# Optimization experiments

Hardware: AMD Instinct MI355X
Metric: run time of the kernel (lower is better)

Reference implementation:

```python
import jax, jax.numpy as jnp
import numpy as np

V = 25; NE = 5; DIM = 192; H = 6; HD = 32; N = 64; T = 64
SCALE = HD ** -0.5
COEFF = 0.4
NTU_EDGES = [(1,2),(2,21),(3,21),(4,3),(5,21),(6,5),(7,6),(8,7),(9,21),(10,9),(11,10),(12,11),(13,1),(14,13),(15,14),(16,15),(17,1),(18,17),(19,18),(20,19),(22,23),(23,8),(24,25),(25,12)]

def _compute_hops():
    # replicate MHSA.__init__ hop-distance computation (A = [I, adj, adj] summed+binarized)
    adj = np.zeros((V, V))
    for i, j in NTU_EDGES:
        adj[i-1, j-1] = 1.0; adj[j-1, i-1] = 1.0
    h1 = ((np.eye(V) + adj) != 0).astype(np.float64)
    h = [None] * V
    h[0] = np.eye(V); h[1] = h1
    hops = np.zeros((V, V))
    for i in range(2, V):
        h[i] = ((h[i-1] @ h1.T) != 0).astype(np.float64)
    for i in range(V-1, 0, -1):
        if np.any(h[i] - h[i-1]):
            h[i] = h[i] - h[i-1]
            hops += i * h[i]
    return hops.astype(np.int32)

def setup_inputs() -> dict:
    key = jax.random.key(0)
    ks = jax.random.split(key, 12)
    hops = jnp.asarray(_compute_hops())
    n_hop = int(hops.max()) + 1
    std = 0.02
    return {
        "x": jax.random.normal(ks[0], (N, DIM, T, V), jnp.float32),
        "joint_label": jnp.arange(V, dtype=jnp.int32) % NE,  # all 5 hyperedge labels present
        "groups": NE,  # unused by forward (kept for signature fidelity)
        "he_weight": jax.random.uniform(ks[1], (NE,), jnp.float32),
        "hops": hops,
        "ln_g": jnp.ones((DIM,), jnp.float32),
        "ln_b": jnp.zeros((DIM,), jnp.float32),
        "hgc_w": std * jax.random.normal(ks[2], (DIM, DIM), jnp.float32),
        "q_w": std * jax.random.normal(ks[3], (DIM, DIM), jnp.float32),
        "kv_w": std * jax.random.normal(ks[4], (2 * DIM, DIM), jnp.float32),
        "proj_w": std * jax.random.normal(ks[5], (DIM, HD), jnp.float32),  # grouped 1x1 conv, groups=6
        "proj_b": jnp.zeros((DIM,), jnp.float32),
        "rpe": std * jax.random.normal(ks[6], (n_hop, DIM), jnp.float32),
        "w1": std * jax.random.normal(ks[7], (H, HD), jnp.float32),
        "outer": jnp.tile(jnp.eye(V, dtype=jnp.float32), (H, 1, 1)) + std * jax.random.normal(ks[8], (H, V, V), jnp.float32),
        "alpha": 0.1 * jnp.ones((1,), jnp.float32),
        "lin1_w": std * jax.random.normal(ks[9], (T // 5, T), jnp.float32),
        "lin1_b": jnp.zeros((T // 5,), jnp.float32),
        "lin2_w": std * jax.random.normal(ks[10], (T, T // 5), jnp.float32),
        "lin2_b": jnp.zeros((T,), jnp.float32),
    }

def _forward(x, joint_label, he_weight, hops, ln_g, ln_b, hgc_w, q_w, kv_w, proj_w, proj_b, rpe, w1, outer, alpha, lin1_w, lin1_b, lin2_w, lin2_b):
    N_, C, T_, V_ = x.shape
    # ---- HGattn branch: hypergraph conv + temporal squeeze-excite gate ----
    label = jax.nn.one_hot(joint_label, NE, dtype=x.dtype)            # (V, 5)
    label1 = label / label.sum(0, keepdims=True)
    label1 = label1 / jnp.sqrt(label.sum(1, keepdims=True))
    label1 = (he_weight[None, :] * label1).T                          # (5, V)
    norm_label = label / label.sum(1, keepdims=True)
    h_adj = norm_label @ label1                                       # (V, V)
    z = jnp.einsum('nctv,vw->nctw', x, h_adj)
    op = jnp.einsum('nctv,oc->notv', z, hgc_w)                        # (N, dim, T, V) 1x1 conv
    op_tr = op.transpose(0, 1, 3, 2)                                  # (N, dim, V, T)
    s = op_tr.mean(axis=(1, 2))                                       # (N, T) global avg pool over (dim, V)
    g = jax.nn.sigmoid(jax.nn.relu(s @ lin1_w.T + lin1_b) @ lin2_w.T + lin2_b)  # (N, T)
    op_final = op_tr + COEFF * (op_tr * g[:, None, None, :])
    e = op_final.transpose(0, 1, 3, 2)                                # (N, dim, T, V)
    # ---- LayerNorm over channel dim ----
    xc = x.transpose(0, 2, 3, 1)                                      # (N, T, V, C)
    mu = xc.mean(-1, keepdims=True)
    var = xc.var(-1, keepdims=True)
    xn = (((xc - mu) / jnp.sqrt(var + 1e-5)) * ln_g + ln_b).transpose(0, 3, 1, 2)
    # ---- MHSA with hop-indexed relative bias, e-branch scores, outer fusion ----
    q = jnp.einsum('nctv,oc->notv', xn, q_w).reshape(N_, H, HD, T_, V_).transpose(0, 3, 1, 4, 2)   # (N,T,H,V,hd)
    kv = jnp.einsum('nctv,oc->notv', xn, kv_w).reshape(N_, 2, H, HD, T_, V_)
    k = kv[:, 0].transpose(0, 3, 1, 4, 2)
    v = kv[:, 1].transpose(0, 3, 1, 4, 2)
    e_k = e.reshape(N_, H, HD, T_, V_).transpose(0, 3, 1, 4, 2)
    k_r = rpe[hops].reshape(V_, V_, H, HD)                            # hop-distance relative position table
    b = jnp.einsum('bthnc,nmhc->bthnm', q, k_r)
    c = jnp.einsum('bthnc,bthmc->bthnm', q, e_k)
    d = jnp.einsum('hc,bthmc->bthm', w1, e_k)[..., None, :]
    a = jnp.einsum('bthnc,bthmc->bthnm', q, k)
    attn = jax.nn.softmax((a + b + c + d) * SCALE, axis=-1)
    o = jnp.einsum('bthnm,bthmc->bthnc', alpha * attn + outer[None, None], v)
    o = o.transpose(0, 1, 2, 4, 3).reshape(N_, T_, DIM, V_).transpose(0, 2, 1, 3)  # (N, dim, T, V)
    # grouped 1x1 conv projection (groups = H)
    og = o.reshape(N_, H, HD, T_, V_)
    wg = proj_w.reshape(H, HD, HD)
    o = jnp.einsum('ngitv,goi->ngotv', og, wg).reshape(N_, DIM, T_, V_) + proj_b[None, :, None, None]
    return x + o  # dim_in == dim -> identity skip

def reference(x, joint_label, groups, he_weight, hops, ln_g, ln_b, hgc_w, q_w, kv_w, proj_w, proj_b, rpe, w1, outer, alpha, lin1_w, lin1_b, lin2_w, lin2_b):
    return _forward(x, joint_label, he_weight, hops, ln_g, ln_b, hgc_w, q_w, kv_w, proj_w, proj_b, rpe, w1, outer, alpha, lin1_w, lin1_b, lin2_w, lin2_b)
```

## Files before the change

### kernel.cpp

```cpp
#include <hip/hip_runtime.h>
#include <hip/hip_bf16.h>

using bf16 = __hip_bfloat16;
typedef __bf16 bf16x8 __attribute__((ext_vector_type(8)));
typedef float f32x4 __attribute__((ext_vector_type(4)));

constexpr int kDim = 192;
constexpr int kH = 6;
constexpr int kHd = 32;
constexpr int kN = 64;
constexpr int kT = 64;
constexpr int kV = 25;
constexpr int kP = kT * kV;
constexpr int kNCstride = kDim * kP;
constexpr float kScale = 0.17677669529663687f;
constexpr float kCoeff = 0.4f;

__global__ void __launch_bounds__(256) setup_kernel(
    const int* __restrict__ jl, const float* __restrict__ hew,
    const float* __restrict__ hgc, const float* __restrict__ qw,
    const float* __restrict__ kvw, const float* __restrict__ rpe,
    const float* __restrict__ proj_w, const float* __restrict__ lng,
    const float* __restrict__ lnb, int n_hop, float* __restrict__ hadj,
    bf16* __restrict__ Wb, float* __restrict__ G, float* __restrict__ Bb,
    bf16* __restrict__ RPEb, bf16* __restrict__ pwb, bf16* __restrict__ VT) {
  const int bid = blockIdx.x;
  const int tid = threadIdx.x;
  if (bid < 576) {
    int i = bid * 256 + tid;
    float v;
    if (i < 36864) {
      v = hgc[i];
    } else {
      int local = i - 36864;
      int c = local % kDim;
      v = (local < 36864) ? qw[local] : kvw[local - 36864];
      v *= lng[c];
    }
    Wb[i] = __float2bfloat16(v);
  } else if (bid == 576) {
    __shared__ int lbl[kV];
    __shared__ int cnt[8];
    if (tid < 8) cnt[tid] = 0;
    __syncthreads();
    if (tid < kV) { lbl[tid] = jl[tid]; atomicAdd(&cnt[lbl[tid]], 1); }
    __syncthreads();
    for (int idx = tid; idx < kV * kV; idx += 256) {
      int v = idx / kV, w = idx - v * kV;
      float val = 0.f;
      if (lbl[v] == lbl[w]) val = hew[lbl[v]] / (float)cnt[lbl[v]];
      hadj[idx] = val;
    }
  } else if (bid == 577) {
    for (int i = tid; i < kH * 16 * kHd; i += 256) {
      int h = i >> 9, hp = (i >> 5) & 15, d = i & 31;
      float v = (hp < n_hop) ? rpe[hp * kDim + h * kHd + d] : 0.f;
      RPEb[i] = __float2bfloat16(v);
    }
    for (int i = tid; i < kDim * kHd; i += 256)
      pwb[i] = __float2bfloat16(proj_w[i]);
  } else if (bid < 722) {
    int o = (bid - 578) * 4 + (tid >> 6);
    int lane = tid & 63;
    const float* Wr =
        (o < kDim) ? (qw + (size_t)o * kDim) : (kvw + (size_t)(o - kDim) * kDim);
    float gs = 0.f, bs = 0.f;
    for (int c = lane; c < kDim; c += 64) {
      float wv = Wr[c];
      gs += wv * lng[c];
      bs += wv * lnb[c];
    }
    for (int off = 32; off > 0; off >>= 1) {
      gs += __shfl_down(gs, off);
      bs += __shfl_down(bs, off);
    }
    if (lane == 0) { G[o] = gs; Bb[o] = bs; }
  } else {
    int row = (bid - 722) * 256 + tid;
    if (row < kN * kT * kDim) {
      uint4 z = {0u, 0u, 0u, 0u};
      *reinterpret_cast<uint4*>(reinterpret_cast<char*>(VT) + (size_t)row * 64 +
                                48) = z;
    }
  }
}

__global__ void __launch_bounds__(256) prep_kernel(
    const float* __restrict__ x, bf16* __restrict__ XR, float* __restrict__ mu,
    float* __restrict__ rstd) {
  __shared__ float ps[kV][25], ps2[kV][25];
  const int tid = threadIdx.x;
  const int t = blockIdx.x, n = blockIdx.y;
  const float* xb = x + (size_t)n * kNCstride + t * kV;
  size_t ob = ((size_t)n * kP + t * kV) * kDim;
  for (int idx = tid; idx < 600; idx += 256) {
    int p = idx % 25, c8 = idx / 25;
    float a = 0.f, b = 0.f;
    union { uint4 u; __bf16 h[8]; } pk;
#pragma unroll
    for (int i = 0; i < 8; ++i) {
      float v = xb[(size_t)(c8 * 8 + i) * kP + p];
      a += v;
      b += v * v;
      pk.h[i] = (__bf16)v;
    }
    *reinterpret_cast<uint4*>(XR + ob + (size_t)p * kDim + c8 * 8) = pk.u;
    ps[p][c8] = a;
    ps2[p][c8] = b;
  }
  __syncthreads();
  if (tid < kV) {
    float a = 0.f, b = 0.f;
#pragma unroll
    for (int c8 = 0; c8 < 24; ++c8) { a += ps[tid][c8]; b += ps2[tid][c8]; }
    float m = a * (1.f / kDim);
    float var = b * (1.f / kDim) - m * m;
    int gid = n * kP + t * kV + tid;
    mu[gid] = m;
    rstd[gid] = rsqrtf(var + 1e-5f);
  }
}

template <int OBN, int MOUT, bool VS, bool LNF>
__global__ void __launch_bounds__(64) mfma_gemm_kernel(
    const bf16* __restrict__ A, const bf16* __restrict__ B,
    bf16* __restrict__ out, bf16* __restrict__ VT,
    const float* __restrict__ muA, const float* __restrict__ rsA,
    const float* __restrict__ G, const float* __restrict__ Bb) {
  int id = blockIdx.x;
  int per = gridDim.x >> 3;
  int wg = (id & 7) * per + (id >> 3);
  int n = wg / (25 * OBN);
  int rem = wg - n * (25 * OBN);
  const int pb = (rem / OBN) * 64;
  const int ob = (rem % OBN) * 64;
  const int l = threadIdx.x;
  B += (size_t)n * kNCstride;
  out += (size_t)n * kP * MOUT;
  f32x4 acc[4][4] = {};
  const int lm = l & 15;
  const int lk = (l >> 4) * 8;
  for (int kb = 0; kb < kDim; kb += 32) {
    bf16x8 af[4], bfv[4];
#pragma unroll
    for (int mf = 0; mf < 4; ++mf)
      af[mf] = *reinterpret_cast<const bf16x8*>(
          A + (size_t)(ob + mf * 16 + lm) * kDim + kb + lk);
#pragma unroll
    for (int nf = 0; nf < 4; ++nf)
      bfv[nf] = *reinterpret_cast<const bf16x8*>(
          B + (size_t)(pb + nf * 16 + lm) * kDim + kb + lk);
#pragma unroll
    for (int mf = 0; mf < 4; ++mf)
#pragma unroll
      for (int nf = 0; nf < 4; ++nf)
        acc[mf][nf] = __builtin_amdgcn_mfma_f32_16x16x32_bf16(
            af[mf], bfv[nf], acc[mf][nf], 0, 0, 0);
  }
  const int r0 = (l >> 4) * 4;
  float rsv[4], muv[4];
  if (LNF) {
#pragma unroll
    for (int nf = 0; nf < 4; ++nf) {
      int p = pb + nf * 16 + lm;
      rsv[nf] = rsA[n * kP + p];
      muv[nf] = muA[n * kP + p];
    }
  }
  int tt[4], vv[4];
#pragma unroll
  for (int nf = 0; nf < 4; ++nf) {
    int p = pb + nf * 16 + lm;
    tt[nf] = p / 25;
    vv[nf] = p - tt[nf] * 25;
  }
#pragma unroll
  for (int mf = 0; mf < 4; ++mf) {
    const int o0 = ob + mf * 16 + r0;
    float ga[4] = {0.f, 0.f, 0.f, 0.f}, ba[4] = {0.f, 0.f, 0.f, 0.f};
    if (LNF) {
      float4 g4 = *reinterpret_cast<const float4*>(G + o0);
      float4 b4 = *reinterpret_cast<const float4*>(Bb + o0);
      ga[0] = g4.x; ga[1] = g4.y; ga[2] = g4.z; ga[3] = g4.w;
      ba[0] = b4.x; ba[1] = b4.y; ba[2] = b4.z; ba[3] = b4.w;
    }
    if (!VS || o0 < 384) {
#pragma unroll
      for (int nf = 0; nf < 4; ++nf) {
        const int p = pb + nf * 16 + lm;
        union { uint2 u; bf16 b[4]; } pk;
#pragma unroll
        for (int r = 0; r < 4; ++r) {
          float vvv = acc[mf][nf][r];
          if (LNF) vvv = rsv[nf] * (vvv - muv[nf] * ga[r]) + ba[r];
          pk.b[r] = __float2bfloat16(vvv);
        }
        *reinterpret_cast<uint2*>(out + (size_t)p * MOUT + o0) = pk.u;
      }
    } else {
#pragma unroll
      for (int nf = 0; nf < 4; ++nf) {
        size_t rowb =
            ((size_t)(n * kT + tt[nf]) * kDim + (o0 - 384)) * 32 + vv[nf];
#pragma unroll
        for (int r = 0; r < 4; ++r) {
          float vvv = acc[mf][nf][r];
          if (LNF) vvv = rsv[nf] * (vvv - muv[nf] * ga[r]) + ba[r];
          VT[rowb + (size_t)r * 32] = __float2bfloat16(vvv);
        }
      }
    }
  }
}

__global__ void __launch_bounds__(256) haapply_kernel(
    bf16* __restrict__ OP, const float* __restrict__ hadjg,
    float* __restrict__ s_out) {
  __shared__ ushort tile[kV * kDim];
  __shared__ float ha[640];
  __shared__ float red[4];
  const int tid = threadIdx.x;
  const int t = blockIdx.x, n = blockIdx.y;
  size_t base = ((size_t)n * kP + t * kV) * kDim;
  for (int i = tid; i < kV * kV; i += 256) ha[i] = hadjg[i];
  const uint2* src = reinterpret_cast<const uint2*>(OP + base);
  uint2* dst2 = reinterpret_cast<uint2*>(tile);
  for (int i = tid; i < kV * kDim / 4; i += 256) dst2[i] = src[i];
  __syncthreads();
  float ssum = 0.f;
  for (int idx = tid; idx < 600; idx += 256) {
    int c8 = idx % 24, w = idx / 24;
    float acc[8] = {0.f, 0.f, 0.f, 0.f, 0.f, 0.f, 0.f, 0.f};
    for (int v = 0; v < kV; ++v) {
      float coef = ha[v * kV + w];
      union { uint4 u; __bf16 h[8]; } ld;
      ld.u = *reinterpret_cast<const uint4*>(tile + v * kDim + c8 * 8);
#pragma unroll
      for (int j = 0; j < 8; ++j) acc[j] += coef * (float)ld.h[j];
    }
    union { uint4 u; __bf16 h[8]; } pk;
    float s8 = 0.f;
#pragma unroll
    for (int j = 0; j < 8; ++j) { pk.h[j] = (__bf16)acc[j]; s8 += acc[j]; }
    *reinterpret_cast<uint4*>(OP + base + (size_t)w * kDim + c8 * 8) = pk.u;
    ssum += s8;
  }
  for (int off = 32; off > 0; off >>= 1) ssum += __shfl_down(ssum, off);
  if ((tid & 63) == 0) red[tid >> 6] = ssum;
  __syncthreads();
  if (tid == 0)
    s_out[n * kT + t] = (red[0] + red[1] + red[2] + red[3]) *
                        (1.f / (float)(kDim * kV));
}

__global__ void gate_kernel(const float* __restrict__ s,
                            const float* __restrict__ w1l,
                            const float* __restrict__ b1,
                            const float* __restrict__ w2l,
                            const float* __restrict__ b2,
                            float* __restrict__ gatef) {
  __shared__ float sh[kT];
  __shared__ float hid[12];
  int n = blockIdx.x, t = threadIdx.x;
  sh[t] = s[n * kT + t];
  __syncthreads();
  if (t < 12) {
    float a = b1[t];
    for (int j = 0; j < kT; ++j) a += sh[j] * w1l[t * kT + j];
    hid[t] = fmaxf(a, 0.f);
  }
  __syncthreads();
  float a = b2[t];
  for (int j = 0; j < 12; ++j) a += hid[j] * w2l[t * 12 + j];
  float g = 1.f / (1.f + __expf(-a));
  gatef[n * kT + t] = 1.f + kCoeff * g;
}

__global__ void __launch_bounds__(384) attn_kernel(
    const bf16* __restrict__ QK, const bf16* __restrict__ VT,
    const bf16* __restrict__ OP, const float* __restrict__ gatef,
    const int* __restrict__ hops, const bf16* __restrict__ RPEb,
    const float* __restrict__ w1, const float* __restrict__ outer,
    const float* __restrict__ alpha_p, const bf16* __restrict__ pwb,
    const float* __restrict__ proj_b, const float* __restrict__ x,
    float* __restrict__ out) {
  __shared__ ushort wls[kH][2560];
  __shared__ int hopsS[kV][32];
  const int tid = threadIdx.x;
  const int lane = tid & 63;
  const int h = tid >> 6;
  const int t = blockIdx.x, n = blockIdx.y;
  const int nt = n * kT + t;
  const int lm = lane & 15, g = lane >> 4;

  for (int i = tid; i < kV * 32; i += 384) {
    int v = i >> 5, w = i & 31;
    hopsS[v][w] = (w < kV) ? hops[v * kV + w] : 0;
  }
  __syncthreads();

  bf16* Pp = (bf16*)&wls[h][0];
  bf16* OLp = (bf16*)&wls[h][1280];
  float* QRp = (float*)&wls[h][1280];

  const float f = gatef[nt];
  const float alpha = alpha_p[0];
  const bf16* Qbase = QK + (size_t)(n * kP + t * kV) * 384;
  const bf16* Ebase = OP + (size_t)(n * kP + t * kV) * kDim;
  const int colO = h * kHd + g * 8;

  bf16x8 qf[2], kf[2], ef[2];
#pragma unroll
  for (int mf = 0; mf < 2; ++mf) {
    const bf16* row = Qbase + (size_t)(mf * 16 + lm) * 384;
    qf[mf] = *reinterpret_cast<const bf16x8*>(row + colO);
    kf[mf] = *reinterpret_cast<const bf16x8*>(row + kDim + colO);
    ef[mf] = *reinterpret_cast<const bf16x8*>(
        Ebase + (size_t)(mf * 16 + lm) * kDim + colO);
  }
  bf16x8 rf = *reinterpret_cast<const bf16x8*>(RPEb + (h * 16 + lm) * kHd + g * 8);

  float w1v[8];
  {
    float4 wa = *reinterpret_cast<const float4*>(w1 + h * kHd + g * 8);
    float4 wb = *reinterpret_cast<const float4*>(w1 + h * kHd + g * 8 + 4);
    w1v[0] = wa.x; w1v[1] = wa.y; w1v[2] = wa.z; w1v[3] = wa.w;
    w1v[4] = wb.x; w1v[5] = wb.y; w1v[6] = wb.z; w1v[7] = wb.w;
  }
  float dt[2];
#pragma unroll
  for (int nf = 0; nf < 2; ++nf) {
    float a = 0.f;
#pragma unroll
    for (int j = 0; j < 8; ++j) a += w1v[j] * (float)ef[nf][j];
    a += __shfl_xor(a, 16);
    a += __shfl_xor(a, 32);
    dt[nf] = f * a;
  }

  bf16x8 kef[2];
#pragma unroll
  for (int nf = 0; nf < 2; ++nf)
#pragma unroll
    for (int j = 0; j < 8; ++j)
      kef[nf][j] = (__bf16)((float)kf[nf][j] + f * (float)ef[nf][j]);

  f32x4 aK[2][2] = {};
  f32x4 aR[2] = {};
#pragma unroll
  for (int mf = 0; mf < 2; ++mf) {
#pragma unroll
    for (int nf = 0; nf < 2; ++nf)
      aK[mf][nf] =
          __builtin_amdgcn_mfma_f32_16x16x32_bf16(qf[mf], kef[nf], aK[mf][nf], 0, 0, 0);
    aR[mf] = __builtin_amdgcn_mfma_f32_16x16x32_bf16(qf[mf], rf, aR[mf], 0, 0, 0);
  }

#pragma unroll
  for (int mf = 0; mf < 2; ++mf)
#pragma unroll
    for (int r = 0; r < 4; ++r)
      QRp[(mf * 16 + g * 4 + r) * 18 + lm] = aR[mf][r];

  const bool w1ok = (lm + 16) < kV;
#pragma unroll
  for (int mf = 0; mf < 2; ++mf) {
#pragma unroll
    for (int r = 0; r < 4; ++r) {
      int v = mf * 16 + g * 4 + r;
      int vc = v < kV ? v : kV - 1;
      int hp0 = hopsS[vc][lm];
      int hp1 = hopsS[vc][lm + 16];
      float s0 = (aK[mf][0][r] + QRp[v * 18 + hp0] + dt[0]) * kScale;
      float s1 = (aK[mf][1][r] + QRp[v * 18 + hp1] + dt[1]) * kScale;
      if (!w1ok) s1 = -3.0e38f;
      float m = fmaxf(s0, s1);
#pragma unroll
      for (int d = 1; d < 16; d <<= 1) m = fmaxf(m, __shfl_xor(m, d));
      float e0 = __expf(s0 - m);
      float e1 = w1ok ? __expf(s1 - m) : 0.f;
      float sum = e0 + e1;
#pragma unroll
      for (int d = 1; d < 16; d <<= 1) sum += __shfl_xor(sum, d);
      float inv = alpha / sum;
      float o0 = outer[h * (kV * kV) + vc * kV + lm];
      float o1 = w1ok ? outer[h * (kV * kV) + vc * kV + lm + 16] : 0.f;
      Pp[v * 40 + lm] = __float2bfloat16(e0 * inv + o0);
      Pp[v * 40 + lm + 16] = __float2bfloat16(w1ok ? e1 * inv + o1 : 0.f);
    }
  }

  bf16x8 pa[2], vb[2];
#pragma unroll
  for (int mf = 0; mf < 2; ++mf)
    pa[mf] = *reinterpret_cast<const bf16x8*>(Pp + (mf * 16 + lm) * 40 + g * 8);
#pragma unroll
  for (int nf = 0; nf < 2; ++nf)
    vb[nf] = *reinterpret_cast<const bf16x8*>(
        VT + ((size_t)(nt * kDim + h * kHd + nf * 16 + lm)) * 32 + g * 8);
  f32x4 aO[2][2] = {};
#pragma unroll
  for (int mf = 0; mf < 2; ++mf)
#pragma unroll
    for (int nf = 0; nf < 2; ++nf)
      aO[mf][nf] =
          __builtin_amdgcn_mfma_f32_16x16x32_bf16(pa[mf], vb[nf], aO[mf][nf], 0, 0, 0);

#pragma unroll
  for (int mf = 0; mf < 2; ++mf)
#pragma unroll
    for (int nf = 0; nf < 2; ++nf)
#pragma unroll
      for (int r = 0; r < 4; ++r)
        OLp[(mf * 16 + g * 4 + r) * 40 + nf * 16 + lm] =
            __float2bfloat16(aO[mf][nf][r]);

  bf16x8 oa[2], pwf[2];
#pragma unroll
  for (int nf = 0; nf < 2; ++nf)
    oa[nf] = *reinterpret_cast<const bf16x8*>(OLp + (nf * 16 + lm) * 40 + g * 8);
#pragma unroll
  for (int mf = 0; mf < 2; ++mf)
    pwf[mf] = *reinterpret_cast<const bf16x8*>(pwb +
        (h * kHd + mf * 16 + lm) * kHd + g * 8);
  f32x4 aF[2][2] = {};
#pragma unroll
  for (int mf = 0; mf < 2; ++mf)
#pragma unroll
    for (int nf = 0; nf < 2; ++nf)
      aF[mf][nf] =
          __builtin_amdgcn_mfma_f32_16x16x32_bf16(pwf[mf], oa[nf], aF[mf][nf], 0, 0, 0);

#pragma unroll
  for (int mf = 0; mf < 2; ++mf) {
#pragma unroll
    for (int r = 0; r < 4; ++r) {
      int oo = mf * 16 + g * 4 + r;
      int c = h * kHd + oo;
      float pbv = proj_b[c];
      size_t gbase = (size_t)n * kNCstride + (size_t)c * kP + t * kV;
#pragma unroll
      for (int nf = 0; nf < 2; ++nf) {
        int v = nf * 16 + lm;
        if (v < kV) out[gbase + v] = x[gbase + v] + aF[mf][nf][r] + pbv;
      }
    }
  }
}

extern "C" void kernel_launch(void* const* d_in, const int* in_sizes, int n_in,
                              void* d_out, int out_size, void* d_ws,
                              size_t ws_size, hipStream_t stream) {
  const float* x = (const float*)d_in[0];
  const int* joint_label = (const int*)d_in[1];
  const float* he_weight = (const float*)d_in[3];
  const int* hops = (const int*)d_in[4];
  const float* ln_g = (const float*)d_in[5];
  const float* ln_b = (const float*)d_in[6];
  const float* hgc_w = (const float*)d_in[7];
  const float* q_w = (const float*)d_in[8];
  const float* kv_w = (const float*)d_in[9];
  const float* proj_w = (const float*)d_in[10];
  const float* proj_b = (const float*)d_in[11];
  const float* rpe = (const float*)d_in[12];
  const float* w1 = (const float*)d_in[13];
  const float* outer = (const float*)d_in[14];
  const float* alpha = (const float*)d_in[15];
  const float* lin1_w = (const float*)d_in[16];
  const float* lin1_b = (const float*)d_in[17];
  const float* lin2_w = (const float*)d_in[18];
  const float* lin2_b = (const float*)d_in[19];
  const int n_hop = in_sizes[12] / kDim;

  char* w = (char*)d_ws;
  bf16* QK = (bf16*)w;
  w += (size_t)kN * kP * 2 * kDim * 2;
  bf16* XR = (bf16*)w;
  w += (size_t)kN * kP * kDim * 2;
  bf16* OP = (bf16*)w;
  w += (size_t)kN * kP * kDim * 2;
  w += 65536;
  bf16* VT = (bf16*)w;
  w += (size_t)kN * kT * kDim * 32 * 2;
  bf16* Wb = (bf16*)w;
  w += (size_t)768 * kDim * 2;
  bf16* RPEb = (bf16*)w;
  w += (size_t)kH * 16 * kHd * 2;
  bf16* pwb = (bf16*)w;
  w += (size_t)kDim * kHd * 2;
  float* hadj = (float*)w;
  w += 1024 * 4;
  float* s_ws = (float*)w;
  w += kN * kT * 4;
  float* gatef = (float*)w;
  w += kN * kT * 4;
  float* mu = (float*)w;
  w += (size_t)kN * kP * 4;
  float* rstd = (float*)w;
  w += (size_t)kN * kP * 4;
  float* G = (float*)w;
  w += 576 * 4;
  float* Bb = (float*)w;
  w += 576 * 4;

  hipLaunchKernelGGL(setup_kernel, dim3(3794), dim3(256), 0, stream,
                     joint_label, he_weight, hgc_w, q_w, kv_w, rpe, proj_w,
                     ln_g, ln_b, n_hop, hadj, Wb, G, Bb, RPEb, pwb, VT);
  hipLaunchKernelGGL(prep_kernel, dim3(kT, kN), dim3(256), 0, stream, x, XR,
                     mu, rstd);
  hipLaunchKernelGGL((mfma_gemm_kernel<3, kDim, false, false>),
                     dim3(25 * 3 * kN), dim3(64), 0, stream, Wb, XR, OP,
                     (bf16*)nullptr, nullptr, nullptr, nullptr, nullptr);
  hipLaunchKernelGGL(haapply_kernel, dim3(kT, kN), dim3(256), 0, stream, OP,
                     hadj, s_ws);
  hipLaunchKernelGGL(gate_kernel, dim3(kN), dim3(kT), 0, stream, s_ws, lin1_w,
                     lin1_b, lin2_w, lin2_b, gatef);
  hipLaunchKernelGGL((mfma_gemm_kernel<9, 384, true, true>),
                     dim3(25 * 9 * kN), dim3(64), 0, stream, Wb + 192 * kDim,
                     XR, QK, VT, mu, rstd, G, Bb);
  hipLaunchKernelGGL(attn_kernel, dim3(kT, kN), dim3(384), 0, stream, QK, VT,
                     OP, gatef, hops, RPEb, w1, outer, alpha, pwb, proj_b, x,
                     (float*)d_out);
}
```

Before: 354.6 us.

## Process two timesteps per attention block and drop shared hops table

Each attention block now handles two consecutive timesteps, so the grid is halved and the RPE, w1 and proj weight fragments are loaded once and reused across both. The shared-memory hops staging and its __syncthreads are removed, and hops are read straight from global memory (cached). LDS row padding changes from 40/18 to 34/17. Per-thread register use roughly doubles, which can lower occupancy, and the uncached-pattern hops reads may cost more than the old LDS lookup.

```diff
diff --git a/kernel.cpp b/kernel.cpp
--- a/kernel.cpp
+++ b/kernel.cpp
@@ -284,42 +284,35 @@
     const float* __restrict__ alpha_p, const bf16* __restrict__ pwb,
     const float* __restrict__ proj_b, const float* __restrict__ x,
     float* __restrict__ out) {
-  __shared__ ushort wls[kH][2560];
-  __shared__ int hopsS[kV][32];
+  __shared__ ushort wls[kH][2][2176];
   const int tid = threadIdx.x;
   const int lane = tid & 63;
   const int h = tid >> 6;
-  const int t = blockIdx.x, n = blockIdx.y;
-  const int nt = n * kT + t;
+  const int t0 = blockIdx.x * 2;
+  const int n = blockIdx.y;
   const int lm = lane & 15, g = lane >> 4;
-
-  for (int i = tid; i < kV * 32; i += 384) {
-    int v = i >> 5, w = i & 31;
-    hopsS[v][w] = (w < kV) ? hops[v * kV + w] : 0;
-  }
-  __syncthreads();
-
-  bf16* Pp = (bf16*)&wls[h][0];
-  bf16* OLp = (bf16*)&wls[h][1280];
-  float* QRp = (float*)&wls[h][1280];
-
-  const float f = gatef[nt];
+  const bool w1ok = (lm + 16) < kV;
   const float alpha = alpha_p[0];
-  const bf16* Qbase = QK + (size_t)(n * kP + t * kV) * 384;
-  const bf16* Ebase = OP + (size_t)(n * kP + t * kV) * kDim;
   const int colO = h * kHd + g * 8;
 
-  bf16x8 qf[2], kf[2], ef[2];
-#pragma unroll
-  for (int mf = 0; mf < 2; ++mf) {
-    const bf16* row = Qbase + (size_t)(mf * 16 + lm) * 384;
-    qf[mf] = *reinterpret_cast<const bf16x8*>(row + colO);
-    kf[mf] = *reinterpret_cast<const bf16x8*>(row + kDim + colO);
-    ef[mf] = *reinterpret_cast<const bf16x8*>(
-        Ebase + (size_t)(mf * 16 + lm) * kDim + colO);
+  float fga[2];
+  bf16x8 qf[2][2], kf[2][2], ef[2][2];
+#pragma unroll
+  for (int tk = 0; tk < 2; ++tk) {
+    const int nt = n * kT + t0 + tk;
+    fga[tk] = gatef[nt];
+    const bf16* Qb = QK + (size_t)(nt * kV) * 384;
+    const bf16* Eb = OP + (size_t)(nt * kV) * kDim;
+#pragma unroll
+    for (int mf = 0; mf < 2; ++mf) {
+      const bf16* row = Qb + (size_t)(mf * 16 + lm) * 384;
+      qf[tk][mf] = *reinterpret_cast<const bf16x8*>(row + colO);
+      kf[tk][mf] = *reinterpret_cast<const bf16x8*>(row + kDim + colO);
+      ef[tk][mf] = *reinterpret_cast<const bf16x8*>(
+          Eb + (size_t)(mf * 16 + lm) * kDim + colO);
+    }
   }
   bf16x8 rf = *reinterpret_cast<const bf16x8*>(RPEb + (h * 16 + lm) * kHd + g * 8);
-
   float w1v[8];
   {
     float4 wa = *reinterpret_cast<const float4*>(w1 + h * kHd + g * 8);
@@ -327,122 +320,158 @@
     w1v[0] = wa.x; w1v[1] = wa.y; w1v[2] = wa.z; w1v[3] = wa.w;
     w1v[4] = wb.x; w1v[5] = wb.y; w1v[6] = wb.z; w1v[7] = wb.w;
   }
-  float dt[2];
-#pragma unroll
-  for (int nf = 0; nf < 2; ++nf) {
-    float a = 0.f;
-#pragma unroll
-    for (int j = 0; j < 8; ++j) a += w1v[j] * (float)ef[nf][j];
-    a += __shfl_xor(a, 16);
-    a += __shfl_xor(a, 32);
-    dt[nf] = f * a;
-  }
-
-  bf16x8 kef[2];
-#pragma unroll
-  for (int nf = 0; nf < 2; ++nf)
-#pragma unroll
-    for (int j = 0; j < 8; ++j)
-      kef[nf][j] = (__bf16)((float)kf[nf][j] + f * (float)ef[nf][j]);
-
-  f32x4 aK[2][2] = {};
-  f32x4 aR[2] = {};
-#pragma unroll
-  for (int mf = 0; mf < 2; ++mf) {
+
+  float dt[2][2];
+  bf16x8 kef[2][2];
+#pragma unroll
+  for (int tk = 0; tk < 2; ++tk) {
+#pragma unroll
+    for (int nf = 0; nf < 2; ++nf) {
+      float a = 0.f;
+#pragma unroll
+      for (int j = 0; j < 8; ++j) a += w1v[j] * (float)ef[tk][nf][j];
+      a += __shfl_xor(a, 16);
+      a += __shfl_xor(a, 32);
+      dt[tk][nf] = fga[tk] * a;
+#pragma unroll
+      for (int j = 0; j < 8; ++j)
+        kef[tk][nf][j] =
+            (__bf16)((float)kf[tk][nf][j] + fga[tk] * (float)ef[tk][nf][j]);
+    }
+  }
+
+  f32x4 aS[2][2][2] = {};
+  f32x4 aR[2][2] = {};
+#pragma unroll
+  for (int tk = 0; tk < 2; ++tk)
+#pragma unroll
+    for (int mf = 0; mf < 2; ++mf) {
+#pragma unroll
+      for (int nf = 0; nf < 2; ++nf)
+        aS[tk][mf][nf] = __builtin_amdgcn_mfma_f32_16x16x32_bf16(
+            qf[tk][mf], kef[tk][nf], aS[tk][mf][nf], 0, 0, 0);
+      aR[tk][mf] = __builtin_amdgcn_mfma_f32_16x16x32_bf16(qf[tk][mf], rf,
+                                                           aR[tk][mf], 0, 0, 0);
+    }
+
+#pragma unroll
+  for (int tk = 0; tk < 2; ++tk) {
+    float* QRp = (float*)&wls[h][tk][1088];
+#pragma unroll
+    for (int mf = 0; mf < 2; ++mf)
+#pragma unroll
+      for (int r = 0; r < 4; ++r)
+        QRp[(mf * 16 + g * 4 + r) * 17 + lm] = aR[tk][mf][r];
+  }
+
+#pragma unroll
+  for (int tk = 0; tk < 2; ++tk) {
+    bf16* Pp = (bf16*)&wls[h][tk][0];
+    float* QRp = (float*)&wls[h][tk][1088];
+#pragma unroll
+    for (int mf = 0; mf < 2; ++mf) {
+#pragma unroll
+      for (int r = 0; r < 4; ++r) {
+        int v = mf * 16 + g * 4 + r;
+        int vc = v < kV ? v : kV - 1;
+        int hp0 = hops[vc * kV + lm];
+        int hp1 = w1ok ? hops[vc * kV + lm + 16] : 0;
+        float s0 = (aS[tk][mf][0][r] + QRp[v * 17 + hp0] + dt[tk][0]) * kScale;
+        float s1 = (aS[tk][mf][1][r] + QRp[v * 17 + hp1] + dt[tk][1]) * kScale;
+        if (!w1ok) s1 = -3.0e38f;
+        float m = fmaxf(s0, s1);
+#pragma unroll
+        for (int d = 1; d < 16; d <<= 1) m = fmaxf(m, __shfl_xor(m, d));
+        float e0 = __expf(s0 - m);
+        float e1 = w1ok ? __expf(s1 - m) : 0.f;
+        float sum = e0 + e1;
+#pragma unroll
+        for (int d = 1; d < 16; d <<= 1) sum += __shfl_xor(sum, d);
+        float inv = alpha / sum;
+        const float* orow = outer + h * (kV * kV) + vc * kV;
+        Pp[v * 34 + lm] = __float2bfloat16(e0 * inv + orow[lm]);
+        Pp[v * 34 + lm + 16] =
+            __float2bfloat16(w1ok ? e1 * inv + orow[lm + 16] : 0.f);
+      }
+    }
+  }
+
+  bf16x8 pa[2][2], vbr[2][2];
+#pragma unroll
+  for (int tk = 0; tk < 2; ++tk) {
+    const int nt = n * kT + t0 + tk;
+    bf16* Pp = (bf16*)&wls[h][tk][0];
+#pragma unroll
+    for (int mf = 0; mf < 2; ++mf)
+      pa[tk][mf] =
+          *reinterpret_cast<const bf16x8*>(Pp + (mf * 16 + lm) * 34 + g * 8);
 #pragma unroll
     for (int nf = 0; nf < 2; ++nf)
-      aK[mf][nf] =
-          __builtin_amdgcn_mfma_f32_16x16x32_bf16(qf[mf], kef[nf], aK[mf][nf], 0, 0, 0);
-    aR[mf] = __builtin_amdgcn_mfma_f32_16x16x32_bf16(qf[mf], rf, aR[mf], 0, 0, 0);
-  }
-
+      vbr[tk][nf] = *reinterpret_cast<const bf16x8*>(
+          VT + ((size_t)(nt * kDim + h * kHd + nf * 16 + lm)) * 32 + g * 8);
+  }
+  f32x4 aO[2][2][2] = {};
+#pragma unroll
+  for (int tk = 0; tk < 2; ++tk)
+#pragma unroll
+    for (int mf = 0; mf < 2; ++mf)
+#pragma unroll
+      for (int nf = 0; nf < 2; ++nf)
+        aO[tk][mf][nf] = __builtin_amdgcn_mfma_f32_16x16x32_bf16(
+            pa[tk][mf], vbr[tk][nf], aO[tk][mf][nf], 0, 0, 0);
+
+#pragma unroll
+  for (int tk = 0; tk < 2; ++tk) {
+    bf16* OLp = (bf16*)&wls[h][tk][1088];
+#pragma unroll
+    for (int mf = 0; mf < 2; ++mf)
+#pragma unroll
+      for (int nf = 0; nf < 2; ++nf)
+#pragma unroll
+        for (int r = 0; r < 4; ++r)
+          OLp[(mf * 16 + g * 4 + r) * 34 + nf * 16 + lm] =
+              __float2bfloat16(aO[tk][mf][nf][r]);
+  }
+  bf16x8 pwf[2];
 #pragma unroll
   for (int mf = 0; mf < 2; ++mf)
-#pragma unroll
-    for (int r = 0; r < 4; ++r)
-      QRp[(mf * 16 + g * 4 + r) * 18 + lm] = aR[mf][r];
-
-  const bool w1ok = (lm + 16) < kV;
-#pragma unroll
-  for (int mf = 0; mf < 2; ++mf) {
-#pragma unroll
-    for (int r = 0; r < 4; ++r) {
-      int v = mf * 16 + g * 4 + r;
-      int vc = v < kV ? v : kV - 1;
-      int hp0 = hopsS[vc][lm];
-      int hp1 = hopsS[vc][lm + 16];
-      float s0 = (aK[mf][0][r] + QRp[v * 18 + hp0] + dt[0]) * kScale;
-      float s1 = (aK[mf][1][r] + QRp[v * 18 + hp1] + dt[1]) * kScale;
-      if (!w1ok) s1 = -3.0e38f;
-      float m = fmaxf(s0, s1);
-#pragma unroll
-      for (int d = 1; d < 16; d <<= 1) m = fmaxf(m, __shfl_xor(m, d));
-      float e0 = __expf(s0 - m);
-      float e1 = w1ok ? __expf(s1 - m) : 0.f;
-      float sum = e0 + e1;
-#pragma unroll
-      for (int d = 1; d < 16; d <<= 1) sum += __shfl_xor(sum, d);
-      float inv = alpha / sum;
-      float o0 = outer[h * (kV * kV) + vc * kV + lm];
-      float o1 = w1ok ? outer[h * (kV * kV) + vc * kV + lm + 16] : 0.f;
-      Pp[v * 40 + lm] = __float2bfloat16(e0 * inv + o0);
-      Pp[v * 40 + lm + 16] = __float2bfloat16(w1ok ? e1 * inv + o1 : 0.f);
-    }
-  }
-
-  bf16x8 pa[2], vb[2];
-#pragma unroll
-  for (int mf = 0; mf < 2; ++mf)
-    pa[mf] = *reinterpret_cast<const bf16x8*>(Pp + (mf * 16 + lm) * 40 + g * 8);
-#pragma unroll
-  for (int nf = 0; nf < 2; ++nf)
-    vb[nf] = *reinterpret_cast<const bf16x8*>(
-        VT + ((size_t)(nt * kDim + h * kHd + nf * 16 + lm)) * 32 + g * 8);
-  f32x4 aO[2][2] = {};
-#pragma unroll
-  for (int mf = 0; mf < 2; ++mf)
+    pwf[mf] = *reinterpret_cast<const bf16x8*>(
+        pwb + (h * kHd + mf * 16 + lm) * kHd + g * 8);
+  bf16x8 oa[2][2];
+#pragma unroll
+  for (int tk = 0; tk < 2; ++tk) {
+    bf16* OLp = (bf16*)&wls[h][tk][1088];
 #pragma unroll
     for (int nf = 0; nf < 2; ++nf)
-      aO[mf][nf] =
-          __builtin_amdgcn_mfma_f32_16x16x32_bf16(pa[mf], vb[nf], aO[mf][nf], 0, 0, 0);
-
-#pragma unroll
-  for (int mf = 0; mf < 2; ++mf)
-#pragma unroll
-    for (int nf = 0; nf < 2; ++nf)
-#pragma unroll
-      for (int r = 0; r < 4; ++r)
-        OLp[(mf * 16 + g * 4 + r) * 40 + nf * 16 + lm] =
-            __float2bfloat16(aO[mf][nf][r]);
-
-  bf16x8 oa[2], pwf[2];
-#pragma unroll
-  for (int nf = 0; nf < 2; ++nf)
-    oa[nf] = *reinterpret_cast<const bf16x8*>(OLp + (nf * 16 + lm) * 40 + g * 8);
-#pragma unroll
-  for (int mf = 0; mf < 2; ++mf)
-    pwf[mf] = *reinterpret_cast<const bf16x8*>(pwb +
-        (h * kHd + mf * 16 + lm) * kHd + g * 8);
-  f32x4 aF[2][2] = {};
-#pragma unroll
-  for (int mf = 0; mf < 2; ++mf)
-#pragma unroll
-    for (int nf = 0; nf < 2; ++nf)
-      aF[mf][nf] =
-          __builtin_amdgcn_mfma_f32_16x16x32_bf16(pwf[mf], oa[nf], aF[mf][nf], 0, 0, 0);
-
-#pragma unroll
-  for (int mf = 0; mf < 2; ++mf) {
-#pragma unroll
-    for (int r = 0; r < 4; ++r) {
-      int oo = mf * 16 + g * 4 + r;
-      int c = h * kHd + oo;
-      float pbv = proj_b[c];
-      size_t gbase = (size_t)n * kNCstride + (size_t)c * kP + t * kV;
-#pragma unroll
-      for (int nf = 0; nf < 2; ++nf) {
-        int v = nf * 16 + lm;
-        if (v < kV) out[gbase + v] = x[gbase + v] + aF[mf][nf][r] + pbv;
+      oa[tk][nf] =
+          *reinterpret_cast<const bf16x8*>(OLp + (nf * 16 + lm) * 34 + g * 8);
+  }
+  f32x4 aF[2][2][2] = {};
+#pragma unroll
+  for (int tk = 0; tk < 2; ++tk)
+#pragma unroll
+    for (int mf = 0; mf < 2; ++mf)
+#pragma unroll
+      for (int nf = 0; nf < 2; ++nf)
+        aF[tk][mf][nf] = __builtin_amdgcn_mfma_f32_16x16x32_bf16(
+            pwf[mf], oa[tk][nf], aF[tk][mf][nf], 0, 0, 0);
+
+#pragma unroll
+  for (int tk = 0; tk < 2; ++tk) {
+    const int t = t0 + tk;
+#pragma unroll
+    for (int mf = 0; mf < 2; ++mf) {
+#pragma unroll
+      for (int r = 0; r < 4; ++r) {
+        int oo = mf * 16 + g * 4 + r;
+        int c = h * kHd + oo;
+        float pbv = proj_b[c];
+        size_t gbase = (size_t)n * kNCstride + (size_t)c * kP + t * kV;
+#pragma unroll
+        for (int nf = 0; nf < 2; ++nf) {
+          int v = nf * 16 + lm;
+          if (v < kV) out[gbase + v] = x[gbase + v] + aF[tk][mf][nf][r] + pbv;
+        }
       }
     }
   }
@@ -518,7 +547,7 @@
   hipLaunchKernelGGL((mfma_gemm_kernel<9, 384, true, true>),
                      dim3(25 * 9 * kN), dim3(64), 0, stream, Wb + 192 * kDim,
                      XR, QK, VT, mu, rstd, G, Bb);
-  hipLaunchKernelGGL(attn_kernel, dim3(kT, kN), dim3(384), 0, stream, QK, VT,
-                     OP, gatef, hops, RPEb, w1, outer, alpha, pwb, proj_b, x,
-                     (float*)d_out);
-}
+  hipLaunchKernelGGL(attn_kernel, dim3(kT / 2, kN), dim3(384), 0, stream, QK,
+                     VT, OP, gatef, hops, RPEb, w1, outer, alpha, pwb, proj_b,
+                     x, (float*)d_out);
+}
```

Measured after the change: 390.6 us. 10.1% more time.
